# Performance work log

Hardware: AMD Instinct MI355X
Metric: run time of the kernel (lower is better)

The kernel has to match this reference:

```python
import jax, jax.numpy as jnp
import numpy as np

V, H_BASE, D, L, K = 32000, 4096, 512, 2, 4
B = 64

def setup_inputs() -> dict:
    key = jax.random.key(0)
    ks = jax.random.split(key, 12)
    s = 0.02
    return {
        "hidden_state": jax.random.normal(ks[0], (B, H_BASE), jnp.float32),
        "in_proj_w": jax.random.normal(ks[1], (D, H_BASE), jnp.float32) * s,
        "in_proj_b": jnp.zeros((D,), jnp.float32),
        "w_ih0": jax.random.normal(ks[2], (3 * D, D), jnp.float32) * s,
        "w_hh0": jax.random.normal(ks[3], (3 * D, D), jnp.float32) * s,
        "b_ih0": jax.random.normal(ks[4], (3 * D,), jnp.float32) * s,
        "b_hh0": jax.random.normal(ks[5], (3 * D,), jnp.float32) * s,
        "w_ih1": jax.random.normal(ks[6], (3 * D, D), jnp.float32) * s,
        "w_hh1": jax.random.normal(ks[7], (3 * D, D), jnp.float32) * s,
        "b_ih1": jax.random.normal(ks[8], (3 * D,), jnp.float32) * s,
        "b_hh1": jax.random.normal(ks[9], (3 * D,), jnp.float32) * s,
        "embed": jax.random.normal(ks[10], (V, D), jnp.float32) * s,
        "out_w": jax.random.normal(ks[11], (V, D), jnp.float32) * s,
    }

def _gru_cell(x, h, w_ih, w_hh, b_ih, b_hh):
    # PyTorch GRU gate order: r, z, n
    gi = x @ w_ih.T + b_ih  # [B, 3D]
    gh = h @ w_hh.T + b_hh
    ir, iz, inn = jnp.split(gi, 3, axis=-1)
    hr, hz, hn = jnp.split(gh, 3, axis=-1)
    r = jax.nn.sigmoid(ir + hr)
    z = jax.nn.sigmoid(iz + hz)
    n = jnp.tanh(inn + r * hn)
    return (1.0 - z) * n + z * h

def reference(hidden_state, in_proj_w, in_proj_b, w_ih0, w_hh0, b_ih0, b_hh0,
              w_ih1, w_hh1, b_ih1, b_hh1, embed, out_w):
    b = hidden_state.shape[0]
    h0 = hidden_state @ in_proj_w.T + in_proj_b  # [B, D]
    h_l0 = h0
    h_l1 = h0
    x = jnp.zeros((b, in_proj_w.shape[0]), hidden_state.dtype)
    all_logits = []
    for _ in range(K):
        h_l0 = _gru_cell(x, h_l0, w_ih0, w_hh0, b_ih0, b_hh0)
        h_l1 = _gru_cell(h_l0, h_l1, w_ih1, w_hh1, b_ih1, b_hh1)
        logits = h_l1 @ out_w.T  # [B, V]
        all_logits.append(logits)
        x = embed[jnp.argmax(logits, axis=-1)]  # greedy next-token embed
    return jnp.stack(all_logits, axis=1)  # [B, K, V]
```

## Files before the change

### kernel.cpp

```cpp
#include <hip/hip_runtime.h>
#include <math.h>


typedef __attribute__((ext_vector_type(8))) short short8;
typedef __attribute__((ext_vector_type(4))) float f32x4;

__device__ __forceinline__ unsigned short f2bf_rne(float x) {
    unsigned u = __float_as_uint(x);
    unsigned r = (u + 0x7fffu + ((u >> 16) & 1u)) >> 16;
    return (unsigned short)r;
}
__device__ __forceinline__ void split2(float x, unsigned short& hi, unsigned short& lo) {
    unsigned u = __float_as_uint(x);
    hi = (unsigned short)(u >> 16);
    float r = x - __uint_as_float(u & 0xffff0000u);
    lo = f2bf_rne(r);
}

__device__ __forceinline__ void store_plane(unsigned short* hiP, unsigned short* loP,
                                            int m, int d, float v) {
    int s = d >> 6, cl = (d >> 3) & 7, e = d & 7;
    int off = m * 512 + s * 64 + ((cl ^ (m & 7)) * 8) + e;
    unsigned short hi, lo; split2(v, hi, lo);
    hiP[off] = hi; loP[off] = lo;
}

__device__ __forceinline__ void gload16(const void* g, void* lds) {
    __builtin_amdgcn_global_load_lds(
        (const __attribute__((address_space(1))) unsigned int*)g,
        (__attribute__((address_space(3))) unsigned int*)lds, 16, 0, 0);
}

#define LDTB 72

template<bool ARGMAX>
__device__ __forceinline__ void mfma_gemm(
    const char* __restrict__ AH, const char* __restrict__ AL, int AstrideB,
    const float* __restrict__ W, int ldbK,
    int n0, int k0, int klen,
    float* __restrict__ C, int ldc,
    unsigned short* AsH, unsigned short* AsL,
    unsigned short* BsH, unsigned short* BsL,
    float* __restrict__ pval, int* __restrict__ pidx, int bx)
{
    const int tid  = threadIdx.x;
    const int wv   = tid >> 6;
    const int lane = tid & 63;
    const int lr   = lane & 15;
    const int lh   = lane >> 4;

    f32x4 acc[4];
#pragma unroll
    for (int i = 0; i < 4; ++i) acc[i] = (f32x4){0.f, 0.f, 0.f, 0.f};

    for (int kk = k0; kk < k0 + klen; kk += 64) {
        {
            int m  = tid >> 3;
            int cp = tid & 7;
            const char* sH = AH + m * AstrideB + kk * 2 + cp * 16;
            const char* sL = AL + m * AstrideB + kk * 2 + cp * 16;
            gload16(sH, (char*)AsH + wv * 1024);
            gload16(sL, (char*)AsL + wv * 1024);
        }
#pragma unroll
        for (int r = 0; r < 4; ++r) {
            int idx = r * 512 + tid;
            int n = idx >> 4;
            int q = idx & 15;
            float4 v = *(const float4*)(W + (n0 + n) * ldbK + kk + q * 4);
            unsigned short h0,h1,h2,h3,l0,l1,l2,l3;
            split2(v.x,h0,l0); split2(v.y,h1,l1); split2(v.z,h2,l2); split2(v.w,h3,l3);
            uint2 ph = make_uint2((unsigned)h0 | ((unsigned)h1 << 16),
                                  (unsigned)h2 | ((unsigned)h3 << 16));
            uint2 pl = make_uint2((unsigned)l0 | ((unsigned)l1 << 16),
                                  (unsigned)l2 | ((unsigned)l3 << 16));
            *(uint2*)(BsH + n * LDTB + q * 4) = ph;
            *(uint2*)(BsL + n * LDTB + q * 4) = pl;
        }
        __syncthreads();

#pragma unroll
        for (int kk2 = 0; kk2 < 2; ++kk2) {
            int aoff = lr * 64 + (((kk2 * 4 + lh) ^ (lr & 7)) * 8);
            short8 ah[4], al[4];
#pragma unroll
            for (int mt = 0; mt < 4; ++mt) {
                ah[mt] = *(const short8*)(AsH + mt * 1024 + aoff);
                al[mt] = *(const short8*)(AsL + mt * 1024 + aoff);
            }
            int boff = (wv * 16 + lr) * LDTB + kk2 * 32 + lh * 8;
            short8 bh = *(const short8*)(BsH + boff);
            short8 bl = *(const short8*)(BsL + boff);
#pragma unroll
            for (int mt = 0; mt < 4; ++mt) {
                acc[mt] = __builtin_amdgcn_mfma_f32_16x16x32_bf16(ah[mt], bh, acc[mt], 0, 0, 0);
                acc[mt] = __builtin_amdgcn_mfma_f32_16x16x32_bf16(ah[mt], bl, acc[mt], 0, 0, 0);
                acc[mt] = __builtin_amdgcn_mfma_f32_16x16x32_bf16(al[mt], bh, acc[mt], 0, 0, 0);
            }
        }
        __syncthreads();
    }

#pragma unroll
    for (int mt = 0; mt < 4; ++mt)
#pragma unroll
        for (int i = 0; i < 4; ++i) {
            int m = mt * 16 + lh * 4 + i;
            C[m * ldc + n0 + wv * 16 + lr] = acc[mt][i];
        }

    if (ARGMAX) {
        float* sv = (float*)AsH;
        int*   sc = (int*)AsL;
#pragma unroll
        for (int mt = 0; mt < 4; ++mt)
#pragma unroll
            for (int i = 0; i < 4; ++i) {
                float v = acc[mt][i];
                int   c = n0 + wv * 16 + lr;
#pragma unroll
                for (int msk = 1; msk < 16; msk <<= 1) {
                    float ov = __shfl_xor(v, msk, 64);
                    int   oc = __shfl_xor(c, msk, 64);
                    if (ov > v || (ov == v && oc < c)) { v = ov; c = oc; }
                }
                if (lr == 0) {
                    int row = mt * 16 + lh * 4 + i;
                    sv[wv * 64 + row] = v;
                    sc[wv * 64 + row] = c;
                }
            }
        __syncthreads();
        if (tid < 64) {
            float v = sv[tid]; int c = sc[tid];
#pragma unroll
            for (int w = 1; w < 8; ++w) {
                float ov = sv[w * 64 + tid]; int oc = sc[w * 64 + tid];
                if (ov > v) { v = ov; c = oc; }
            }
            pval[bx * 64 + tid] = v;
            pidx[bx * 64 + tid] = c;
        }
    }
}

#define DECLARE_LDS() \
    __shared__ alignas(16) unsigned short AsH[64 * 64]; \
    __shared__ alignas(16) unsigned short AsL[64 * 64]; \
    __shared__ alignas(16) unsigned short BsH[128 * LDTB]; \
    __shared__ alignas(16) unsigned short BsL[128 * LDTB];

__global__ __launch_bounds__(256) void k_split_A(
    const float* __restrict__ hidden, char* __restrict__ hidH, char* __restrict__ hidL)
{
    int g = blockIdx.x * 256 + threadIdx.x;
    int m = g >> 9;
    int cc = g & 511;
    int s = cc >> 3, cl = cc & 7;
    const float* src = hidden + m * 4096 + cc * 8;
    float4 v0 = *(const float4*)src;
    float4 v1 = *(const float4*)(src + 4);
    unsigned short h[8], l[8];
    split2(v0.x,h[0],l[0]); split2(v0.y,h[1],l[1]); split2(v0.z,h[2],l[2]); split2(v0.w,h[3],l[3]);
    split2(v1.x,h[4],l[4]); split2(v1.y,h[5],l[5]); split2(v1.z,h[6],l[6]); split2(v1.w,h[7],l[7]);
    uint4 ph = make_uint4((unsigned)h[0]|((unsigned)h[1]<<16), (unsigned)h[2]|((unsigned)h[3]<<16),
                          (unsigned)h[4]|((unsigned)h[5]<<16), (unsigned)h[6]|((unsigned)h[7]<<16));
    uint4 pl = make_uint4((unsigned)l[0]|((unsigned)l[1]<<16), (unsigned)l[2]|((unsigned)l[3]<<16),
                          (unsigned)l[4]|((unsigned)l[5]<<16), (unsigned)l[6]|((unsigned)l[7]<<16));
    int off = m * 8192 + s * 128 + ((cl ^ (m & 7)) * 16);
    *(uint4*)(hidH + off) = ph;
    *(uint4*)(hidL + off) = pl;
}

__global__ __launch_bounds__(512) void k_inproj(
    const char* __restrict__ hidH, const char* __restrict__ hidL,
    const float* __restrict__ W, float* __restrict__ part)
{
    DECLARE_LDS();
    int nt = blockIdx.x & 3;
    int ks = blockIdx.x >> 2;
    mfma_gemm<false>(hidH, hidL, 8192, W, 4096, nt * 128, ks * 512, 512,
                     part + ks * 32768, 512, AsH, AsL, BsH, BsL, nullptr, nullptr, 0);
}

__global__ __launch_bounds__(256) void k_reduce_inproj(
    const float* __restrict__ part, const float* __restrict__ bias,
    float* __restrict__ hA, float* __restrict__ hB,
    unsigned short* hAH, unsigned short* hAL,
    unsigned short* hBH, unsigned short* hBL,
    unsigned short* xH,  unsigned short* xL)
{
    int i = blockIdx.x * 256 + threadIdx.x;
    int b = i >> 9;
    int d = i & 511;
    float s = bias[d];
#pragma unroll
    for (int ks = 0; ks < 8; ++ks) s += part[ks * 32768 + i];
    hA[i] = s;
    hB[i] = s;
    store_plane(hAH, hAL, b, d, s);
    store_plane(hBH, hBL, b, d, s);
    store_plane(xH,  xL,  b, d, 0.f);
}

__global__ __launch_bounds__(512) void k_gates(
    const char* __restrict__ xH, const char* __restrict__ xL,
    const char* __restrict__ hH, const char* __restrict__ hL,
    const float* __restrict__ w_ih, const float* __restrict__ w_hh,
    float* __restrict__ gip, float* __restrict__ ghp)
{
    DECLARE_LDS();
    int bx = blockIdx.x;
    int nt = bx % 12;
    int ks = (bx / 12) & 1;
    int mat = bx / 24;
    const char* AH = mat ? hH : xH;
    const char* AL = mat ? hL : xL;
    const float* W = mat ? w_hh : w_ih;
    float* C = (mat ? ghp : gip) + ks * 98304;
    mfma_gemm<false>(AH, AL, 1024, W, 512, nt * 128, ks * 256, 256, C, 1536,
                     AsH, AsL, BsH, BsL, nullptr, nullptr, 0);
}

__global__ __launch_bounds__(256) void k_combine(
    const float* __restrict__ gip, const float* __restrict__ ghp,
    const float* __restrict__ b_ih, const float* __restrict__ b_hh,
    float* __restrict__ h, unsigned short* hH, unsigned short* hL)
{
    int i = blockIdx.x * 256 + threadIdx.x;
    int b = i >> 9;
    int d = i & 511;
    int base = b * 1536 + d;
    float ir = gip[base]         + gip[98304 + base]         + b_ih[d];
    float iz = gip[base + 512]   + gip[98304 + base + 512]   + b_ih[d + 512];
    float inn= gip[base + 1024]  + gip[98304 + base + 1024]  + b_ih[d + 1024];
    float hr = ghp[base]         + ghp[98304 + base]         + b_hh[d];
    float hz = ghp[base + 512]   + ghp[98304 + base + 512]   + b_hh[d + 512];
    float hn = ghp[base + 1024]  + ghp[98304 + base + 1024]  + b_hh[d + 1024];
    float r = 1.f / (1.f + expf(-(ir + hr)));
    float z = 1.f / (1.f + expf(-(iz + hz)));
    float n = tanhf(inn + r * hn);
    float hv = (1.f - z) * n + z * h[i];
    h[i] = hv;
    store_plane(hH, hL, b, d, hv);
}

__global__ __launch_bounds__(512) void k_logits(
    const char* __restrict__ hH, const char* __restrict__ hL,
    const float* __restrict__ W, float* __restrict__ out, int step,
    float* __restrict__ pval, int* __restrict__ pidx)
{
    DECLARE_LDS();
    mfma_gemm<true>(hH, hL, 1024, W, 512, blockIdx.x * 128, 0, 512,
                    out + step * 32000, 128000, AsH, AsL, BsH, BsL,
                    pval, pidx, blockIdx.x);
}

__global__ __launch_bounds__(256) void k_reduce_embed(
    const float* __restrict__ pval, const int* __restrict__ pidx,
    const float* __restrict__ embed, unsigned short* xH, unsigned short* xL)
{
    __shared__ float sv[256];
    __shared__ int   sc[256];
    const int b = blockIdx.x;
    const int tid = threadIdx.x;
    float v = -3.4e38f;
    int   c = 0x7fffffff;
    if (tid < 250) { v = pval[tid * 64 + b]; c = pidx[tid * 64 + b]; }
    sv[tid] = v; sc[tid] = c;
    __syncthreads();
    for (int s = 128; s > 0; s >>= 1) {
        if (tid < s) {
            float ov = sv[tid + s]; int oc = sc[tid + s];
            if (ov > sv[tid] || (ov == sv[tid] && oc < sc[tid])) { sv[tid] = ov; sc[tid] = oc; }
        }
        __syncthreads();
    }
    int tok = sc[0];
    for (int j = tid; j < 512; j += 256)
        store_plane(xH, xL, b, j, embed[tok * 512 + j]);
}

extern "C" void kernel_launch(void* const* d_in, const int* in_sizes, int n_in,
                              void* d_out, int out_size, void* d_ws, size_t ws_size,
                              hipStream_t stream)
{
    const float* hidden = (const float*)d_in[0];
    const float* in_w   = (const float*)d_in[1];
    const float* in_b   = (const float*)d_in[2];
    const float* w_ih0  = (const float*)d_in[3];
    const float* w_hh0  = (const float*)d_in[4];
    const float* b_ih0  = (const float*)d_in[5];
    const float* b_hh0  = (const float*)d_in[6];
    const float* w_ih1  = (const float*)d_in[7];
    const float* w_hh1  = (const float*)d_in[8];
    const float* b_ih1  = (const float*)d_in[9];
    const float* b_hh1  = (const float*)d_in[10];
    const float* embed  = (const float*)d_in[11];
    const float* out_w  = (const float*)d_in[12];
    float* out = (float*)d_out;
    char*  ws  = (char*)d_ws;

    float* hA  = (float*)(ws + 0);
    float* hB  = (float*)(ws + 131072);
    unsigned short* xH  = (unsigned short*)(ws + 262144);
    unsigned short* xL  = (unsigned short*)(ws + 327680);
    unsigned short* hAH = (unsigned short*)(ws + 393216);
    unsigned short* hAL = (unsigned short*)(ws + 458752);
    unsigned short* hBH = (unsigned short*)(ws + 524288);
    unsigned short* hBL = (unsigned short*)(ws + 589824);
    char* hidH = ws + 655360;
    char* hidL = ws + 1179648;
    float* gip = (float*)(ws + 1703936);
    float* ghp = (float*)(ws + 2490368);
    float* ipart = gip;
    float* pval = (float*)(ws + 3276800);
    int*   pidx = (int*)  (ws + 3340800);

    k_split_A<<<128, 256, 0, stream>>>(hidden, hidH, hidL);
    k_inproj<<<32, 512, 0, stream>>>(hidH, hidL, in_w, ipart);
    k_reduce_inproj<<<128, 256, 0, stream>>>(ipart, in_b, hA, hB,
                                             hAH, hAL, hBH, hBL, xH, xL);

    for (int step = 0; step < 4; ++step) {
        k_gates<<<48, 512, 0, stream>>>((char*)xH, (char*)xL, (char*)hAH, (char*)hAL,
                                        w_ih0, w_hh0, gip, ghp);
        k_combine<<<128, 256, 0, stream>>>(gip, ghp, b_ih0, b_hh0, hA, hAH, hAL);
        k_gates<<<48, 512, 0, stream>>>((char*)hAH, (char*)hAL, (char*)hBH, (char*)hBL,
                                        w_ih1, w_hh1, gip, ghp);
        k_combine<<<128, 256, 0, stream>>>(gip, ghp, b_ih1, b_hh1, hB, hBH, hBL);
        k_logits<<<250, 512, 0, stream>>>((char*)hBH, (char*)hBL, out_w, out, step, pval, pidx);
        k_reduce_embed<<<64, 256, 0, stream>>>(pval, pidx, embed, xH, xL);
    }
}
```

Measured before the change: 384.8 us.

## Fuse all stages into one persistent cooperative kernel with grid syncs

Replaces the sequence of 27 separate kernel launches with a single cooperative persistent kernel of 256 blocks that uses grid-wide barriers between stages. The gate GEMMs are also split four ways along K instead of two, giving 96 blocks per gate stage instead of 48. The aim is to remove launch overhead and raise parallelism in the small GRU GEMMs. In exchange it pays for many grid.sync barriers, uses a fixed grid size, and needs a larger workspace for the extra partial sums.

```diff
diff --git a/kernel.cpp b/kernel.cpp
--- a/kernel.cpp
+++ b/kernel.cpp
@@ -1,5 +1,8 @@
 #include <hip/hip_runtime.h>
+#include <hip/hip_cooperative_groups.h>
 #include <math.h>
+
+namespace cg = cooperative_groups;
 
 
 typedef __attribute__((ext_vector_type(8))) short short8;
@@ -141,102 +144,41 @@
             pval[bx * 64 + tid] = v;
             pidx[bx * 64 + tid] = c;
         }
-    }
-}
-
-#define DECLARE_LDS() \
-    __shared__ alignas(16) unsigned short AsH[64 * 64]; \
-    __shared__ alignas(16) unsigned short AsL[64 * 64]; \
-    __shared__ alignas(16) unsigned short BsH[128 * LDTB]; \
-    __shared__ alignas(16) unsigned short BsL[128 * LDTB];
-
-__global__ __launch_bounds__(256) void k_split_A(
-    const float* __restrict__ hidden, char* __restrict__ hidH, char* __restrict__ hidL)
-{
-    int g = blockIdx.x * 256 + threadIdx.x;
-    int m = g >> 9;
-    int cc = g & 511;
-    int s = cc >> 3, cl = cc & 7;
-    const float* src = hidden + m * 4096 + cc * 8;
-    float4 v0 = *(const float4*)src;
-    float4 v1 = *(const float4*)(src + 4);
-    unsigned short h[8], l[8];
-    split2(v0.x,h[0],l[0]); split2(v0.y,h[1],l[1]); split2(v0.z,h[2],l[2]); split2(v0.w,h[3],l[3]);
-    split2(v1.x,h[4],l[4]); split2(v1.y,h[5],l[5]); split2(v1.z,h[6],l[6]); split2(v1.w,h[7],l[7]);
-    uint4 ph = make_uint4((unsigned)h[0]|((unsigned)h[1]<<16), (unsigned)h[2]|((unsigned)h[3]<<16),
-                          (unsigned)h[4]|((unsigned)h[5]<<16), (unsigned)h[6]|((unsigned)h[7]<<16));
-    uint4 pl = make_uint4((unsigned)l[0]|((unsigned)l[1]<<16), (unsigned)l[2]|((unsigned)l[3]<<16),
-                          (unsigned)l[4]|((unsigned)l[5]<<16), (unsigned)l[6]|((unsigned)l[7]<<16));
-    int off = m * 8192 + s * 128 + ((cl ^ (m & 7)) * 16);
-    *(uint4*)(hidH + off) = ph;
-    *(uint4*)(hidL + off) = pl;
-}
-
-__global__ __launch_bounds__(512) void k_inproj(
-    const char* __restrict__ hidH, const char* __restrict__ hidL,
-    const float* __restrict__ W, float* __restrict__ part)
-{
-    DECLARE_LDS();
-    int nt = blockIdx.x & 3;
-    int ks = blockIdx.x >> 2;
-    mfma_gemm<false>(hidH, hidL, 8192, W, 4096, nt * 128, ks * 512, 512,
-                     part + ks * 32768, 512, AsH, AsL, BsH, BsL, nullptr, nullptr, 0);
-}
-
-__global__ __launch_bounds__(256) void k_reduce_inproj(
-    const float* __restrict__ part, const float* __restrict__ bias,
-    float* __restrict__ hA, float* __restrict__ hB,
-    unsigned short* hAH, unsigned short* hAL,
-    unsigned short* hBH, unsigned short* hBL,
-    unsigned short* xH,  unsigned short* xL)
-{
-    int i = blockIdx.x * 256 + threadIdx.x;
-    int b = i >> 9;
-    int d = i & 511;
-    float s = bias[d];
-#pragma unroll
-    for (int ks = 0; ks < 8; ++ks) s += part[ks * 32768 + i];
-    hA[i] = s;
-    hB[i] = s;
-    store_plane(hAH, hAL, b, d, s);
-    store_plane(hBH, hBL, b, d, s);
-    store_plane(xH,  xL,  b, d, 0.f);
-}
-
-__global__ __launch_bounds__(512) void k_gates(
-    const char* __restrict__ xH, const char* __restrict__ xL,
-    const char* __restrict__ hH, const char* __restrict__ hL,
-    const float* __restrict__ w_ih, const float* __restrict__ w_hh,
-    float* __restrict__ gip, float* __restrict__ ghp)
-{
-    DECLARE_LDS();
-    int bx = blockIdx.x;
-    int nt = bx % 12;
-    int ks = (bx / 12) & 1;
-    int mat = bx / 24;
-    const char* AH = mat ? hH : xH;
-    const char* AL = mat ? hL : xL;
-    const float* W = mat ? w_hh : w_ih;
-    float* C = (mat ? ghp : gip) + ks * 98304;
-    mfma_gemm<false>(AH, AL, 1024, W, 512, nt * 128, ks * 256, 256, C, 1536,
-                     AsH, AsL, BsH, BsL, nullptr, nullptr, 0);
-}
-
-__global__ __launch_bounds__(256) void k_combine(
-    const float* __restrict__ gip, const float* __restrict__ ghp,
-    const float* __restrict__ b_ih, const float* __restrict__ b_hh,
-    float* __restrict__ h, unsigned short* hH, unsigned short* hL)
-{
-    int i = blockIdx.x * 256 + threadIdx.x;
+        __syncthreads();
+    }
+}
+
+struct Params {
+    const float *hidden, *in_w, *in_b;
+    const float *w_ih0, *w_hh0, *b_ih0, *b_hh0;
+    const float *w_ih1, *w_hh1, *b_ih1, *b_hh1;
+    const float *embed, *out_w;
+    float* out;
+    char *hidH, *hidL;
+    float* ipart;
+    float *hA, *hB;
+    unsigned short *xH, *xL, *hAH, *hAL, *hBH, *hBL;
+    float *gip, *ghp;
+    float* pval; int* pidx;
+};
+
+__device__ __forceinline__ void combine_elem(
+    int i, const float* gip, const float* ghp,
+    const float* b_ih, const float* b_hh,
+    float* h, unsigned short* hH, unsigned short* hL)
+{
     int b = i >> 9;
     int d = i & 511;
     int base = b * 1536 + d;
-    float ir = gip[base]         + gip[98304 + base]         + b_ih[d];
-    float iz = gip[base + 512]   + gip[98304 + base + 512]   + b_ih[d + 512];
-    float inn= gip[base + 1024]  + gip[98304 + base + 1024]  + b_ih[d + 1024];
-    float hr = ghp[base]         + ghp[98304 + base]         + b_hh[d];
-    float hz = ghp[base + 512]   + ghp[98304 + base + 512]   + b_hh[d + 512];
-    float hn = ghp[base + 1024]  + ghp[98304 + base + 1024]  + b_hh[d + 1024];
+    float ir = b_ih[d], iz = b_ih[d + 512], inn = b_ih[d + 1024];
+    float hr = b_hh[d], hz = b_hh[d + 512], hn = b_hh[d + 1024];
+#pragma unroll
+    for (int s = 0; s < 4; ++s) {
+        const float* g = gip + s * 98304 + base;
+        const float* q = ghp + s * 98304 + base;
+        ir += g[0]; iz += g[512]; inn += g[1024];
+        hr += q[0]; hz += q[512]; hn += q[1024];
+    }
     float r = 1.f / (1.f + expf(-(ir + hr)));
     float z = 1.f / (1.f + expf(-(iz + hz)));
     float n = tanhf(inn + r * hn);
@@ -245,91 +187,160 @@
     store_plane(hH, hL, b, d, hv);
 }
 
-__global__ __launch_bounds__(512) void k_logits(
-    const char* __restrict__ hH, const char* __restrict__ hL,
-    const float* __restrict__ W, float* __restrict__ out, int step,
-    float* __restrict__ pval, int* __restrict__ pidx)
-{
-    DECLARE_LDS();
-    mfma_gemm<true>(hH, hL, 1024, W, 512, blockIdx.x * 128, 0, 512,
-                    out + step * 32000, 128000, AsH, AsL, BsH, BsL,
-                    pval, pidx, blockIdx.x);
-}
-
-__global__ __launch_bounds__(256) void k_reduce_embed(
-    const float* __restrict__ pval, const int* __restrict__ pidx,
-    const float* __restrict__ embed, unsigned short* xH, unsigned short* xL)
-{
-    __shared__ float sv[256];
-    __shared__ int   sc[256];
-    const int b = blockIdx.x;
+__device__ __forceinline__ void gates_task(
+    int t,
+    const unsigned short* xH, const unsigned short* xL,
+    const unsigned short* hH, const unsigned short* hL,
+    const float* w_ih, const float* w_hh,
+    float* gip, float* ghp,
+    unsigned short* AsH, unsigned short* AsL,
+    unsigned short* BsH, unsigned short* BsL)
+{
+    int mat = t / 48;
+    int ks  = (t / 12) & 3;
+    int nt  = t % 12;
+    const char* AH = (const char*)(mat ? hH : xH);
+    const char* AL = (const char*)(mat ? hL : xL);
+    const float* W = mat ? w_hh : w_ih;
+    float* C = (mat ? ghp : gip) + ks * 98304;
+    mfma_gemm<false>(AH, AL, 1024, W, 512, nt * 128, ks * 128, 128, C, 1536,
+                     AsH, AsL, BsH, BsL, nullptr, nullptr, 0);
+}
+
+__global__ __launch_bounds__(512, 2) void k_persist(Params p)
+{
+    __shared__ alignas(16) unsigned short AsH[64 * 64];
+    __shared__ alignas(16) unsigned short AsL[64 * 64];
+    __shared__ alignas(16) unsigned short BsH[128 * LDTB];
+    __shared__ alignas(16) unsigned short BsL[128 * LDTB];
+
+    cg::grid_group grid = cg::this_grid();
+    const int bx  = blockIdx.x;
     const int tid = threadIdx.x;
-    float v = -3.4e38f;
-    int   c = 0x7fffffff;
-    if (tid < 250) { v = pval[tid * 64 + b]; c = pidx[tid * 64 + b]; }
-    sv[tid] = v; sc[tid] = c;
-    __syncthreads();
-    for (int s = 128; s > 0; s >>= 1) {
-        if (tid < s) {
-            float ov = sv[tid + s]; int oc = sc[tid + s];
-            if (ov > sv[tid] || (ov == sv[tid] && oc < sc[tid])) { sv[tid] = ov; sc[tid] = oc; }
-        }
-        __syncthreads();
-    }
-    int tok = sc[0];
-    for (int j = tid; j < 512; j += 256)
-        store_plane(xH, xL, b, j, embed[tok * 512 + j]);
+    const int gtid = bx * 512 + tid;
+
+    if (gtid < 32768) {
+        int m = gtid >> 9;
+        int cc = gtid & 511;
+        int s = cc >> 3, cl = cc & 7;
+        const float* src = p.hidden + m * 4096 + cc * 8;
+        float4 v0 = *(const float4*)src;
+        float4 v1 = *(const float4*)(src + 4);
+        unsigned short h[8], l[8];
+        split2(v0.x,h[0],l[0]); split2(v0.y,h[1],l[1]); split2(v0.z,h[2],l[2]); split2(v0.w,h[3],l[3]);
+        split2(v1.x,h[4],l[4]); split2(v1.y,h[5],l[5]); split2(v1.z,h[6],l[6]); split2(v1.w,h[7],l[7]);
+        uint4 ph = make_uint4((unsigned)h[0]|((unsigned)h[1]<<16), (unsigned)h[2]|((unsigned)h[3]<<16),
+                              (unsigned)h[4]|((unsigned)h[5]<<16), (unsigned)h[6]|((unsigned)h[7]<<16));
+        uint4 pl = make_uint4((unsigned)l[0]|((unsigned)l[1]<<16), (unsigned)l[2]|((unsigned)l[3]<<16),
+                              (unsigned)l[4]|((unsigned)l[5]<<16), (unsigned)l[6]|((unsigned)l[7]<<16));
+        int off = m * 8192 + s * 128 + ((cl ^ (m & 7)) * 16);
+        *(uint4*)(p.hidH + off) = ph;
+        *(uint4*)(p.hidL + off) = pl;
+    }
+    grid.sync();
+
+    if (bx < 32) {
+        int nt = bx & 3, ks = bx >> 2;
+        mfma_gemm<false>(p.hidH, p.hidL, 8192, p.in_w, 4096, nt * 128, ks * 512, 512,
+                         p.ipart + ks * 32768, 512, AsH, AsL, BsH, BsL, nullptr, nullptr, 0);
+    }
+    grid.sync();
+
+    if (gtid < 32768) {
+        int b = gtid >> 9, d = gtid & 511;
+        float s = p.in_b[d];
+#pragma unroll
+        for (int ks = 0; ks < 8; ++ks) s += p.ipart[ks * 32768 + gtid];
+        p.hA[gtid] = s;
+        p.hB[gtid] = s;
+        store_plane(p.hAH, p.hAL, b, d, s);
+        store_plane(p.hBH, p.hBL, b, d, s);
+        store_plane(p.xH,  p.xL,  b, d, 0.f);
+    }
+    grid.sync();
+
+    for (int step = 0; step < 4; ++step) {
+        if (bx < 96)
+            gates_task(bx, p.xH, p.xL, p.hAH, p.hAL, p.w_ih0, p.w_hh0,
+                       p.gip, p.ghp, AsH, AsL, BsH, BsL);
+        grid.sync();
+        if (gtid < 32768)
+            combine_elem(gtid, p.gip, p.ghp, p.b_ih0, p.b_hh0, p.hA, p.hAH, p.hAL);
+        grid.sync();
+        if (bx < 96)
+            gates_task(bx, p.hAH, p.hAL, p.hBH, p.hBL, p.w_ih1, p.w_hh1,
+                       p.gip, p.ghp, AsH, AsL, BsH, BsL);
+        grid.sync();
+        if (gtid < 32768)
+            combine_elem(gtid, p.gip, p.ghp, p.b_ih1, p.b_hh1, p.hB, p.hBH, p.hBL);
+        grid.sync();
+        if (bx < 250)
+            mfma_gemm<true>((const char*)p.hBH, (const char*)p.hBL, 1024,
+                            p.out_w, 512, bx * 128, 0, 512,
+                            p.out + step * 32000, 128000,
+                            AsH, AsL, BsH, BsL, p.pval, p.pidx, bx);
+        grid.sync();
+        if (bx < 64) {
+            float* sv = (float*)AsH;
+            int*   sc = (int*)AsL;
+            if (tid < 256) {
+                float v = -3.4e38f; int c = 0x7fffffff;
+                if (tid < 250) { v = p.pval[tid * 64 + bx]; c = p.pidx[tid * 64 + bx]; }
+                sv[tid] = v; sc[tid] = c;
+            }
+            __syncthreads();
+            for (int s = 128; s > 0; s >>= 1) {
+                if (tid < s) {
+                    float ov = sv[tid + s]; int oc = sc[tid + s];
+                    if (ov > sv[tid] || (ov == sv[tid] && oc < sc[tid])) { sv[tid] = ov; sc[tid] = oc; }
+                }
+                __syncthreads();
+            }
+            int tok = sc[0];
+            store_plane(p.xH, p.xL, bx, tid, p.embed[tok * 512 + tid]);
+        }
+        grid.sync();
+    }
 }
 
 extern "C" void kernel_launch(void* const* d_in, const int* in_sizes, int n_in,
                               void* d_out, int out_size, void* d_ws, size_t ws_size,
                               hipStream_t stream)
 {
-    const float* hidden = (const float*)d_in[0];
-    const float* in_w   = (const float*)d_in[1];
-    const float* in_b   = (const float*)d_in[2];
-    const float* w_ih0  = (const float*)d_in[3];
-    const float* w_hh0  = (const float*)d_in[4];
-    const float* b_ih0  = (const float*)d_in[5];
-    const float* b_hh0  = (const float*)d_in[6];
-    const float* w_ih1  = (const float*)d_in[7];
-    const float* w_hh1  = (const float*)d_in[8];
-    const float* b_ih1  = (const float*)d_in[9];
-    const float* b_hh1  = (const float*)d_in[10];
-    const float* embed  = (const float*)d_in[11];
-    const float* out_w  = (const float*)d_in[12];
-    float* out = (float*)d_out;
-    char*  ws  = (char*)d_ws;
-
-    float* hA  = (float*)(ws + 0);
-    float* hB  = (float*)(ws + 131072);
-    unsigned short* xH  = (unsigned short*)(ws + 262144);
-    unsigned short* xL  = (unsigned short*)(ws + 327680);
-    unsigned short* hAH = (unsigned short*)(ws + 393216);
-    unsigned short* hAL = (unsigned short*)(ws + 458752);
-    unsigned short* hBH = (unsigned short*)(ws + 524288);
-    unsigned short* hBL = (unsigned short*)(ws + 589824);
-    char* hidH = ws + 655360;
-    char* hidL = ws + 1179648;
-    float* gip = (float*)(ws + 1703936);
-    float* ghp = (float*)(ws + 2490368);
-    float* ipart = gip;
-    float* pval = (float*)(ws + 3276800);
-    int*   pidx = (int*)  (ws + 3340800);
-
-    k_split_A<<<128, 256, 0, stream>>>(hidden, hidH, hidL);
-    k_inproj<<<32, 512, 0, stream>>>(hidH, hidL, in_w, ipart);
-    k_reduce_inproj<<<128, 256, 0, stream>>>(ipart, in_b, hA, hB,
-                                             hAH, hAL, hBH, hBL, xH, xL);
-
-    for (int step = 0; step < 4; ++step) {
-        k_gates<<<48, 512, 0, stream>>>((char*)xH, (char*)xL, (char*)hAH, (char*)hAL,
-                                        w_ih0, w_hh0, gip, ghp);
-        k_combine<<<128, 256, 0, stream>>>(gip, ghp, b_ih0, b_hh0, hA, hAH, hAL);
-        k_gates<<<48, 512, 0, stream>>>((char*)hAH, (char*)hAL, (char*)hBH, (char*)hBL,
-                                        w_ih1, w_hh1, gip, ghp);
-        k_combine<<<128, 256, 0, stream>>>(gip, ghp, b_ih1, b_hh1, hB, hBH, hBL);
-        k_logits<<<250, 512, 0, stream>>>((char*)hBH, (char*)hBL, out_w, out, step, pval, pidx);
-        k_reduce_embed<<<64, 256, 0, stream>>>(pval, pidx, embed, xH, xL);
-    }
-}
+    char* ws = (char*)d_ws;
+    Params p;
+    p.hidden = (const float*)d_in[0];
+    p.in_w   = (const float*)d_in[1];
+    p.in_b   = (const float*)d_in[2];
+    p.w_ih0  = (const float*)d_in[3];
+    p.w_hh0  = (const float*)d_in[4];
+    p.b_ih0  = (const float*)d_in[5];
+    p.b_hh0  = (const float*)d_in[6];
+    p.w_ih1  = (const float*)d_in[7];
+    p.w_hh1  = (const float*)d_in[8];
+    p.b_ih1  = (const float*)d_in[9];
+    p.b_hh1  = (const float*)d_in[10];
+    p.embed  = (const float*)d_in[11];
+    p.out_w  = (const float*)d_in[12];
+    p.out    = (float*)d_out;
+
+    p.hidH = ws + 0;
+    p.hidL = ws + 524288;
+    p.ipart= (float*)(ws + 1048576);
+    p.hA   = (float*)(ws + 2097152);
+    p.hB   = (float*)(ws + 2228224);
+    p.xH   = (unsigned short*)(ws + 2359296);
+    p.xL   = (unsigned short*)(ws + 2424832);
+    p.hAH  = (unsigned short*)(ws + 2490368);
+    p.hAL  = (unsigned short*)(ws + 2555904);
+    p.hBH  = (unsigned short*)(ws + 2621440);
+    p.hBL  = (unsigned short*)(ws + 2686976);
+    p.gip  = (float*)(ws + 2752512);
+    p.ghp  = (float*)(ws + 4325376);
+    p.pval = (float*)(ws + 5898240);
+    p.pidx = (int*)  (ws + 5962240);
+
+    void* kp[] = { (void*)&p };
+    hipLaunchCooperativeKernel((const void*)k_persist, dim3(256), dim3(512),
+                               kp, 0, stream);
+}
```

After: 1.117 ms. +190.2%, slower.
